# Kernel optimization log

Measured on AMD Instinct MI355X. Metric: run time of the kernel, lower is better.

Reference implementation:

```python
import jax, jax.numpy as jnp
import numpy as np

EPS = 1e-8  # torch.nn.CosineSimilarity default eps


def _cosine_sim(a, b):
    # cosine similarity along channel dim (axis=1), matching torch semantics:
    # dot / (max(||a||, eps) * max(||b||, eps))
    na = jnp.maximum(jnp.sqrt(jnp.sum(a * a, axis=1)), EPS)
    nb = jnp.maximum(jnp.sqrt(jnp.sum(b * b, axis=1)), EPS)
    return jnp.sum(a * b, axis=1) / (na * nb)  # [B, T]


def setup_inputs() -> dict:
    key = jax.random.key(0)
    k1, k2, k3 = jax.random.split(key, 3)
    B, C, T, O, K = 8, 512, 4096, 512, 3
    feature = jax.random.normal(k1, (B, C, T), dtype=jnp.float32)
    embedding = jax.random.normal(k2, (B, C, T), dtype=jnp.float32)
    weight = jax.random.normal(k3, (O, C, K), dtype=jnp.float32) * 0.05
    return {"feature": feature, "embedding": embedding, "weight": weight}


def reference(feature, embedding, weight):
    B, C, T = feature.shape
    O = weight.shape[0]
    K = 3  # kernel_size is structurally 3 in this module

    # shifted embeddings with zero padding (left / right neighbors)
    emb_l = jnp.pad(embedding[:, :, :-1], ((0, 0), (0, 0), (1, 0)))
    emb_r = jnp.pad(embedding[:, :, 1:], ((0, 0), (0, 0), (0, 1)))
    sim = jnp.stack(
        [_cosine_sim(embedding, emb_l),
         _cosine_sim(embedding, embedding),
         _cosine_sim(embedding, emb_r)],
        axis=1,
    )  # [B, 3, T]

    # tile: first C rows = sim_l, next C = sim_c, last C = sim_r -> [B, 3C, T]
    att = jnp.repeat(sim, C, axis=1)

    # im2col (nn.Unfold with kernel (3,1), padding (1,0)): channel-major layout
    f_pad = jnp.pad(feature, ((0, 0), (0, 0), (1, 1)))  # [B, C, T+2]
    inp_unf = jnp.stack([f_pad[:, :, k:k + T] for k in range(K)], axis=2)
    inp_unf = inp_unf.reshape(B, C * K, T)  # row index = c*3 + k (torch unfold order)

    w_flat = weight.reshape(O, C * K)
    # out[b,o,t] = sum_i (inp_unf * att)[b,i,t] * w_flat[o,i]
    out = jnp.einsum('bit,oi->bot', inp_unf * att, w_flat)
    return out
```

## Files before the change

### kernel.cpp

```cpp
#include <hip/hip_runtime.h>
#include <hip/hip_bf16.h>
#include <stdint.h>

#define B_ 8
#define C_ 512
#define T_ 4096
#define O_ 512
#define KP_ 1728
#define EPS_ 1e-8f

#define BM 256
#define BN 128
#define FTP_ROWS 4104

#define LDS_A_USH 16384
#define LDS_B_USH 8192
#define LDS_BUF_USH 24576
#define LDS_BYTES (3 * LDS_BUF_USH * 2)

typedef unsigned short ushort_t;
typedef __attribute__((ext_vector_type(4))) float f32x4;
typedef __attribute__((ext_vector_type(8))) short bf16x8;

__device__ __forceinline__ ushort_t f2bf(float f) {
  union { float f; uint32_t u; } x; x.f = f;
  uint32_t u = x.u;
  uint32_t r = (u + 0x7FFFu + ((u >> 16) & 1u)) >> 16;
  return (ushort_t)r;
}

#define GLOAD16(gsrc, ldst) \
  __builtin_amdgcn_global_load_lds((const __attribute__((address_space(1))) unsigned int*)(gsrc), \
                                   (__attribute__((address_space(3))) unsigned int*)(ldst), 16, 0, 0)

__global__ void sim_reduce_kernel(const float* __restrict__ emb,
                                  float* __restrict__ nn_out,
                                  float* __restrict__ dl_out) {
  const int b = blockIdx.y;
  const int t0 = (blockIdx.x * 64 + threadIdx.x) * 4;
  const int cty = threadIdx.y;
  float nn0=0.f,nn1=0.f,nn2=0.f,nn3=0.f;
  float dl0=0.f,dl1=0.f,dl2=0.f,dl3=0.f;
  const float* base = emb + (size_t)b * C_ * T_;
  for (int c = cty * 128; c < cty * 128 + 128; ++c) {
    const float* row = base + (size_t)c * T_;
    float4 v = *(const float4*)(row + t0);
    float el = (t0 > 0) ? row[t0 - 1] : 0.f;
    nn0 += v.x*v.x; nn1 += v.y*v.y; nn2 += v.z*v.z; nn3 += v.w*v.w;
    dl0 += v.x*el;  dl1 += v.y*v.x; dl2 += v.z*v.y; dl3 += v.w*v.z;
  }
  __shared__ float red[4][64*8];
  float* myr = &red[cty][threadIdx.x * 8];
  if (cty != 0) {
    myr[0]=nn0; myr[1]=nn1; myr[2]=nn2; myr[3]=nn3;
    myr[4]=dl0; myr[5]=dl1; myr[6]=dl2; myr[7]=dl3;
  }
  __syncthreads();
  if (cty == 0) {
    for (int q = 1; q < 4; ++q) {
      float* r = &red[q][threadIdx.x * 8];
      nn0+=r[0]; nn1+=r[1]; nn2+=r[2]; nn3+=r[3];
      dl0+=r[4]; dl1+=r[5]; dl2+=r[6]; dl3+=r[7];
    }
    float* nb = nn_out + (size_t)b * T_ + t0;
    float* db = dl_out + (size_t)b * T_ + t0;
    nb[0]=nn0; nb[1]=nn1; nb[2]=nn2; nb[3]=nn3;
    db[0]=dl0; db[1]=dl1; db[2]=dl2; db[3]=dl3;
  }
}

__global__ void sim_finalize_kernel(const float* __restrict__ nn,
                                    const float* __restrict__ dl,
                                    float* __restrict__ sim) {
  const int idx = blockIdx.x * 256 + threadIdx.x;
  if (idx >= B_ * T_) return;
  const int b = idx >> 12;
  const int t = idx & (T_ - 1);
  const float* nnb = nn + (size_t)b * T_;
  const float* dlb = dl + (size_t)b * T_;
  float nncur = nnb[t];
  float ncur = fmaxf(sqrtf(nncur), EPS_);
  float sc = nncur / (ncur * ncur);
  float sl = 0.f, sr = 0.f;
  if (t > 0) {
    float np = fmaxf(sqrtf(nnb[t - 1]), EPS_);
    sl = dlb[t] / (ncur * np);
  }
  if (t < T_ - 1) {
    float nx = fmaxf(sqrtf(nnb[t + 1]), EPS_);
    sr = dlb[t + 1] / (ncur * nx);
  }
  float* simb = sim + (size_t)b * 3 * T_;
  simb[t] = sl;
  simb[T_ + t] = sc;
  simb[2 * T_ + t] = sr;
}

__global__ void wperm_kernel(const float* __restrict__ w, ushort_t* __restrict__ wbf) {
  const int idx = blockIdx.x * 256 + threadIdx.x;
  if (idx >= O_ * KP_) return;
  const int o = idx / KP_;
  const int p = idx - o * KP_;
  const int g = p / 576; const int r = p - g * 576;
  const int k = r / 192; const int j = r - k * 192;
  const int c_lo = (512 * g - k + 2) / 3;
  const int c_hi = (512 * g + 511 - k) / 3;
  const int c = (c_lo & ~7) + j;
  float v = (c >= c_lo && c <= c_hi) ? w[((size_t)o * C_ + c) * 3 + k] : 0.f;
  wbf[idx] = f2bf(v);
}

__global__ void zero_pads_kernel(ushort_t* __restrict__ Ftp) {
  const int b = blockIdx.x;
  const int rsel = blockIdx.y;
  const int row = (rsel == 0) ? 0 : (rsel == 1 ? T_ + 1 : T_ + 2);
  uint4* dst = (uint4*)(Ftp + ((size_t)b * FTP_ROWS + row) * 512);
  if (threadIdx.x < 64) dst[threadIdx.x] = make_uint4(0, 0, 0, 0);
}

__global__ void transpose_kernel(const float* __restrict__ feat, ushort_t* __restrict__ Ftp) {
  const int b = blockIdx.z;
  const int c0 = blockIdx.y * 64;
  const int t0 = blockIdx.x * 64;
  __shared__ ushort_t LT[64 * 72];
  const int tid = threadIdx.x;
  {
    const int cl = tid >> 2;
    const int tq = (tid & 3) * 16;
    const float* src = feat + ((size_t)b * C_ + c0 + cl) * T_ + t0 + tq;
    for (int q = 0; q < 4; ++q) {
      float4 v = *(const float4*)(src + q * 4);
      const int t = tq + q * 4;
      LT[(t + 0) * 72 + cl] = f2bf(v.x);
      LT[(t + 1) * 72 + cl] = f2bf(v.y);
      LT[(t + 2) * 72 + cl] = f2bf(v.z);
      LT[(t + 3) * 72 + cl] = f2bf(v.w);
    }
  }
  __syncthreads();
  {
    const int tl = tid >> 2;
    const int cq = (tid & 3) * 16;
    ushort_t* dst = Ftp + ((size_t)b * FTP_ROWS + t0 + tl + 1) * 512 + c0 + cq;
    *(uint4*)(dst) = *(const uint4*)&LT[tl * 72 + cq];
    *(uint4*)(dst + 8) = *(const uint4*)&LT[tl * 72 + cq + 8];
  }
}

__global__ __launch_bounds__(512, 2)
void conv_gemm_kernel(const ushort_t* __restrict__ Ftp,
                      const ushort_t* __restrict__ wbf,
                      const float* __restrict__ sim,
                      float* __restrict__ out) {
  extern __shared__ ushort_t lds[];

  const int b = blockIdx.z;
  const int oBase = blockIdx.y * BM;
  const int tBase = blockIdx.x * BN;

  const int tid = threadIdx.x;
  const int lane = tid & 63;
  const int wid = tid >> 6;
  const int wm = wid >> 1;
  const int wn = wid & 1;
  const int llo = lane & 15, lhi = lane >> 4;

  const int rbase = wid * 8 + (lane >> 3);
  const int sw = (((lane & 7) ^ ((lane >> 3) & 7)) << 3);

  const ushort_t* ftpB = Ftp + (size_t)b * FTP_ROWS * 512;
  const float* simB = sim + (size_t)b * 3 * T_;

  float sv[3][4];
#pragma unroll
  for (int g = 0; g < 3; ++g)
#pragma unroll
    for (int n = 0; n < 4; ++n) {
      sv[g][n] = simB[g * T_ + tBase + wn * 64 + n * 16 + llo];
      asm volatile("" : "+v"(sv[g][n]));
    }

  f32x4 cacc[4][4], oacc[4][4];
  const f32x4 vzero = {0.f, 0.f, 0.f, 0.f};
#pragma unroll
  for (int m = 0; m < 4; ++m)
#pragma unroll
    for (int n = 0; n < 4; ++n) { cacc[m][n] = vzero; oacc[m][n] = vzero; }

  auto STAGE = [&](int s2, int p) {
    const int g = s2 / 9, r = s2 - g * 9, k = r / 3, jb = r - k * 3;
    const int c_lo = (512 * g - k + 2) / 3;
    const int c_st = c_lo & ~7;
    const ushort_t* aS = wbf + (size_t)(oBase + rbase) * KP_ + s2 * 64 + sw;
    const ushort_t* bS = ftpB + (size_t)(tBase + rbase + k) * 512 + c_st + jb * 64 + sw;
    ushort_t* Ad = lds + p * LDS_BUF_USH + wid * 512;
    ushort_t* Bd = lds + p * LDS_BUF_USH + LDS_A_USH + wid * 512;
#pragma unroll
    for (int i = 0; i < 4; ++i)
      GLOAD16(aS + (size_t)i * 64 * KP_, Ad + i * 4096);
#pragma unroll
    for (int i = 0; i < 2; ++i)
      GLOAD16(bS + (size_t)i * 64 * 512, Bd + i * 4096);
  };

  STAGE(0, 0); STAGE(1, 1); STAGE(2, 2);

#pragma unroll
  for (int s = 0; s < 27; ++s) {
    if (s <= 24)      { asm volatile("s_waitcnt vmcnt(12)" ::: "memory"); }
    else if (s == 25) { asm volatile("s_waitcnt vmcnt(6)" ::: "memory"); }
    else              { asm volatile("s_waitcnt vmcnt(0)" ::: "memory"); }
    __builtin_amdgcn_s_barrier();
    asm volatile("" ::: "memory");

    const int p = s % 3;
    const ushort_t* As = lds + p * LDS_BUF_USH;
    const ushort_t* Bs = As + LDS_A_USH;
#pragma unroll
    for (int h = 0; h < 2; ++h) {
      bf16x8 af[4], bfv[4];
#pragma unroll
      for (int m = 0; m < 4; ++m) {
        const int row = wm * 64 + m * 16 + llo;
        af[m] = *(const bf16x8*)&As[row * 64 + (((h * 4 + lhi) ^ (llo & 7)) << 3)];
      }
#pragma unroll
      for (int n = 0; n < 4; ++n) {
        const int row = wn * 64 + n * 16 + llo;
        bfv[n] = *(const bf16x8*)&Bs[row * 64 + (((h * 4 + lhi) ^ (llo & 7)) << 3)];
      }
      __builtin_amdgcn_s_setprio(1);
#pragma unroll
      for (int m = 0; m < 4; ++m)
#pragma unroll
        for (int n = 0; n < 4; ++n)
          cacc[m][n] = __builtin_amdgcn_mfma_f32_16x16x32_bf16(af[m], bfv[n], cacc[m][n], 0, 0, 0);
      __builtin_amdgcn_s_setprio(0);
    }

    __builtin_amdgcn_sched_barrier(0);
    asm volatile("" ::: "memory");
    __builtin_amdgcn_s_barrier();
    asm volatile("" ::: "memory");

    if (s + 3 < 27) STAGE(s + 3, p);

    if (s == 8 || s == 17 || s == 26) {
      const int g = s / 9;
#pragma unroll
      for (int n = 0; n < 4; ++n) {
        const float sc = sv[g][n];
#pragma unroll
        for (int m = 0; m < 4; ++m) {
          oacc[m][n] += sc * cacc[m][n];
          cacc[m][n] = vzero;
        }
      }
    }
  }

  float* outB = out + ((size_t)b * O_ + oBase) * T_ + tBase;
#pragma unroll
  for (int m = 0; m < 4; ++m) {
    const int r0 = wm * 64 + m * 16 + lhi * 4;
#pragma unroll
    for (int n = 0; n < 4; ++n) {
      const int cg = wn * 64 + n * 16 + llo;
#pragma unroll
      for (int r = 0; r < 4; ++r)
        outB[(size_t)(r0 + r) * T_ + cg] = oacc[m][n][r];
    }
  }
}

extern "C" void kernel_launch(void* const* d_in, const int* in_sizes, int n_in,
                              void* d_out, int out_size, void* d_ws, size_t ws_size,
                              hipStream_t stream) {
  const float* feature   = (const float*)d_in[0];
  const float* embedding = (const float*)d_in[1];
  const float* weight    = (const float*)d_in[2];
  float* out = (float*)d_out;

  float* ws  = (float*)d_ws;
  float* nn  = ws;
  float* dl  = nn + (size_t)B_ * T_;
  float* sim = dl + (size_t)B_ * T_;
  ushort_t* wbf = (ushort_t*)(sim + (size_t)3 * B_ * T_);
  ushort_t* Ftp = wbf + (size_t)O_ * KP_;

  (void)hipFuncSetAttribute((const void*)conv_gemm_kernel,
                            hipFuncAttributeMaxDynamicSharedMemorySize, LDS_BYTES);

  zero_pads_kernel<<<dim3(B_, 3), 64, 0, stream>>>(Ftp);
  sim_reduce_kernel<<<dim3(T_ / 256, B_), dim3(64, 4), 0, stream>>>(embedding, nn, dl);
  sim_finalize_kernel<<<dim3((B_ * T_) / 256), 256, 0, stream>>>(nn, dl, sim);
  wperm_kernel<<<dim3((O_ * KP_ + 255) / 256), 256, 0, stream>>>(weight, wbf);
  transpose_kernel<<<dim3(T_ / 64, C_ / 64, B_), 256, 0, stream>>>(feature, Ftp);
  conv_gemm_kernel<<<dim3(T_ / BN, O_ / BM, B_), 512, LDS_BYTES, stream>>>(Ftp, wbf, sim, out);
}
```

Measured before the change: 118.0 us.

## Split GEMM stages into half-K ring buffer with single barrier, merge prep kernels

The conv GEMM main loop now stages half-K (32-wide) slices into a 4-slot LDS ring instead of full 64-wide slices in 3 buffers. Each phase issues the next global-to-LDS prefetch right after its fragment reads and needs only one barrier, so loads overlap with MFMA and synchronisation stalls shrink. The swizzle is re-derived for 32-column rows. The sim finalize and weight permute kernels are merged into one launch, and pad zeroing moves into extra transpose blocks, cutting launch count. The risks are more barriers per K step and LDS bank conflicts under the new swizzle.

Result: faster. 115.4 us (-2.2%).

```diff
diff --git a/kernel.cpp b/kernel.cpp
--- a/kernel.cpp
+++ b/kernel.cpp
@@ -13,10 +13,8 @@
 #define BN 128
 #define FTP_ROWS 4104
 
-#define LDS_A_USH 16384
-#define LDS_B_USH 8192
-#define LDS_BUF_USH 24576
-#define LDS_BYTES (3 * LDS_BUF_USH * 2)
+#define RING_USH 12288
+#define LDS_BYTES (4 * RING_USH * 2)
 
 typedef unsigned short ushort_t;
 typedef __attribute__((ext_vector_type(4))) float f32x4;
@@ -69,61 +67,60 @@
   }
 }
 
-__global__ void sim_finalize_kernel(const float* __restrict__ nn,
-                                    const float* __restrict__ dl,
-                                    float* __restrict__ sim) {
-  const int idx = blockIdx.x * 256 + threadIdx.x;
-  if (idx >= B_ * T_) return;
-  const int b = idx >> 12;
-  const int t = idx & (T_ - 1);
-  const float* nnb = nn + (size_t)b * T_;
-  const float* dlb = dl + (size_t)b * T_;
-  float nncur = nnb[t];
-  float ncur = fmaxf(sqrtf(nncur), EPS_);
-  float sc = nncur / (ncur * ncur);
-  float sl = 0.f, sr = 0.f;
-  if (t > 0) {
-    float np = fmaxf(sqrtf(nnb[t - 1]), EPS_);
-    sl = dlb[t] / (ncur * np);
-  }
-  if (t < T_ - 1) {
-    float nx = fmaxf(sqrtf(nnb[t + 1]), EPS_);
-    sr = dlb[t + 1] / (ncur * nx);
-  }
-  float* simb = sim + (size_t)b * 3 * T_;
-  simb[t] = sl;
-  simb[T_ + t] = sc;
-  simb[2 * T_ + t] = sr;
-}
-
-__global__ void wperm_kernel(const float* __restrict__ w, ushort_t* __restrict__ wbf) {
-  const int idx = blockIdx.x * 256 + threadIdx.x;
-  if (idx >= O_ * KP_) return;
-  const int o = idx / KP_;
-  const int p = idx - o * KP_;
-  const int g = p / 576; const int r = p - g * 576;
-  const int k = r / 192; const int j = r - k * 192;
-  const int c_lo = (512 * g - k + 2) / 3;
-  const int c_hi = (512 * g + 511 - k) / 3;
-  const int c = (c_lo & ~7) + j;
-  float v = (c >= c_lo && c <= c_hi) ? w[((size_t)o * C_ + c) * 3 + k] : 0.f;
-  wbf[idx] = f2bf(v);
-}
-
-__global__ void zero_pads_kernel(ushort_t* __restrict__ Ftp) {
-  const int b = blockIdx.x;
-  const int rsel = blockIdx.y;
-  const int row = (rsel == 0) ? 0 : (rsel == 1 ? T_ + 1 : T_ + 2);
-  uint4* dst = (uint4*)(Ftp + ((size_t)b * FTP_ROWS + row) * 512);
-  if (threadIdx.x < 64) dst[threadIdx.x] = make_uint4(0, 0, 0, 0);
+__global__ void prep_small_kernel(const float* __restrict__ nn,
+                                  const float* __restrict__ dl,
+                                  float* __restrict__ sim,
+                                  const float* __restrict__ w,
+                                  ushort_t* __restrict__ wbf) {
+  const int bid = blockIdx.x;
+  if (bid < 128) {
+    const int idx = bid * 256 + threadIdx.x;
+    const int b = idx >> 12;
+    const int t = idx & (T_ - 1);
+    const float* nnb = nn + (size_t)b * T_;
+    const float* dlb = dl + (size_t)b * T_;
+    float nncur = nnb[t];
+    float ncur = fmaxf(sqrtf(nncur), EPS_);
+    float sc = nncur / (ncur * ncur);
+    float sl = 0.f, sr = 0.f;
+    if (t > 0) {
+      float np = fmaxf(sqrtf(nnb[t - 1]), EPS_);
+      sl = dlb[t] / (ncur * np);
+    }
+    if (t < T_ - 1) {
+      float nx = fmaxf(sqrtf(nnb[t + 1]), EPS_);
+      sr = dlb[t + 1] / (ncur * nx);
+    }
+    float* simb = sim + (size_t)b * 3 * T_;
+    simb[t] = sl;
+    simb[T_ + t] = sc;
+    simb[2 * T_ + t] = sr;
+  } else {
+    const int idx = (bid - 128) * 256 + threadIdx.x;
+    if (idx >= O_ * KP_) return;
+    const int o = idx / KP_;
+    const int p = idx - o * KP_;
+    const int g = p / 576; const int r = p - g * 576;
+    const int k = r / 192; const int j = r - k * 192;
+    const int c_lo = (512 * g - k + 2) / 3;
+    const int c_hi = (512 * g + 511 - k) / 3;
+    const int c = (c_lo & ~7) + j;
+    float v = (c >= c_lo && c <= c_hi) ? w[((size_t)o * C_ + c) * 3 + k] : 0.f;
+    wbf[idx] = f2bf(v);
+  }
 }
 
 __global__ void transpose_kernel(const float* __restrict__ feat, ushort_t* __restrict__ Ftp) {
   const int b = blockIdx.z;
   const int c0 = blockIdx.y * 64;
+  const int tid = threadIdx.x;
+  if (blockIdx.x == T_ / 64) {
+    if (tid < 64)        Ftp[((size_t)b * FTP_ROWS + 0) * 512 + c0 + tid] = 0;
+    else if (tid < 128)  Ftp[((size_t)b * FTP_ROWS + T_ + 1) * 512 + c0 + (tid - 64)] = 0;
+    return;
+  }
   const int t0 = blockIdx.x * 64;
   __shared__ ushort_t LT[64 * 72];
-  const int tid = threadIdx.x;
   {
     const int cl = tid >> 2;
     const int tq = (tid & 3) * 16;
@@ -165,8 +162,10 @@
   const int wn = wid & 1;
   const int llo = lane & 15, lhi = lane >> 4;
 
-  const int rbase = wid * 8 + (lane >> 3);
-  const int sw = (((lane & 7) ^ ((lane >> 3) & 7)) << 3);
+  const int rdsw = ((lhi ^ ((llo >> 1) & 3)) << 3);
+  const int gch = ((lane & 3) ^ ((lane >> 3) & 3)) << 3;
+  const int arow = wid * 32 + (lane >> 2);
+  const int brow = wid * 16 + (lane >> 2);
 
   const ushort_t* ftpB = Ftp + (size_t)b * FTP_ROWS * 512;
   const float* simB = sim + (size_t)b * 3 * T_;
@@ -179,6 +178,7 @@
       sv[g][n] = simB[g * T_ + tBase + wn * 64 + n * 16 + llo];
       asm volatile("" : "+v"(sv[g][n]));
     }
+  asm volatile("s_waitcnt vmcnt(0)" ::: "memory");
 
   f32x4 cacc[4][4], oacc[4][4];
   const f32x4 vzero = {0.f, 0.f, 0.f, 0.f};
@@ -187,64 +187,56 @@
 #pragma unroll
     for (int n = 0; n < 4; ++n) { cacc[m][n] = vzero; oacc[m][n] = vzero; }
 
-  auto STAGE = [&](int s2, int p) {
+  auto STAGE = [&](int u) {
+    const int s2 = u >> 1, h = u & 1;
     const int g = s2 / 9, r = s2 - g * 9, k = r / 3, jb = r - k * 3;
-    const int c_lo = (512 * g - k + 2) / 3;
-    const int c_st = c_lo & ~7;
-    const ushort_t* aS = wbf + (size_t)(oBase + rbase) * KP_ + s2 * 64 + sw;
-    const ushort_t* bS = ftpB + (size_t)(tBase + rbase + k) * 512 + c_st + jb * 64 + sw;
-    ushort_t* Ad = lds + p * LDS_BUF_USH + wid * 512;
-    ushort_t* Bd = lds + p * LDS_BUF_USH + LDS_A_USH + wid * 512;
-#pragma unroll
-    for (int i = 0; i < 4; ++i)
-      GLOAD16(aS + (size_t)i * 64 * KP_, Ad + i * 4096);
-#pragma unroll
-    for (int i = 0; i < 2; ++i)
-      GLOAD16(bS + (size_t)i * 64 * 512, Bd + i * 4096);
+    const int c_st = ((512 * g - k + 2) / 3) & ~7;
+    ushort_t* ring = lds + (u & 3) * RING_USH;
+    const ushort_t* aS = wbf + (size_t)(oBase + arow) * KP_ + s2 * 64 + h * 32 + gch;
+    GLOAD16(aS, ring + wid * 1024);
+    GLOAD16(aS + (size_t)16 * KP_, ring + wid * 1024 + 512);
+    const ushort_t* bS = ftpB + (size_t)(tBase + brow + k) * 512 + c_st + jb * 64 + h * 32 + gch;
+    GLOAD16(bS, ring + 8192 + wid * 512);
   };
 
-  STAGE(0, 0); STAGE(1, 1); STAGE(2, 2);
-
-#pragma unroll
-  for (int s = 0; s < 27; ++s) {
-    if (s <= 24)      { asm volatile("s_waitcnt vmcnt(12)" ::: "memory"); }
-    else if (s == 25) { asm volatile("s_waitcnt vmcnt(6)" ::: "memory"); }
+  auto PHASE = [&](int u, int vm) {
+    if (vm == 6)      { asm volatile("s_waitcnt vmcnt(6)" ::: "memory"); }
+    else if (vm == 3) { asm volatile("s_waitcnt vmcnt(3)" ::: "memory"); }
     else              { asm volatile("s_waitcnt vmcnt(0)" ::: "memory"); }
     __builtin_amdgcn_s_barrier();
     asm volatile("" ::: "memory");
 
-    const int p = s % 3;
-    const ushort_t* As = lds + p * LDS_BUF_USH;
-    const ushort_t* Bs = As + LDS_A_USH;
-#pragma unroll
-    for (int h = 0; h < 2; ++h) {
-      bf16x8 af[4], bfv[4];
-#pragma unroll
-      for (int m = 0; m < 4; ++m) {
-        const int row = wm * 64 + m * 16 + llo;
-        af[m] = *(const bf16x8*)&As[row * 64 + (((h * 4 + lhi) ^ (llo & 7)) << 3)];
-      }
-#pragma unroll
-      for (int n = 0; n < 4; ++n) {
-        const int row = wn * 64 + n * 16 + llo;
-        bfv[n] = *(const bf16x8*)&Bs[row * 64 + (((h * 4 + lhi) ^ (llo & 7)) << 3)];
-      }
-      __builtin_amdgcn_s_setprio(1);
-#pragma unroll
-      for (int m = 0; m < 4; ++m)
-#pragma unroll
-        for (int n = 0; n < 4; ++n)
-          cacc[m][n] = __builtin_amdgcn_mfma_f32_16x16x32_bf16(af[m], bfv[n], cacc[m][n], 0, 0, 0);
-      __builtin_amdgcn_s_setprio(0);
-    }
-
+    const ushort_t* Ah = lds + (u & 3) * RING_USH;
+    const ushort_t* Bh = Ah + 8192;
+    bf16x8 af[4], bfv[4];
+#pragma unroll
+    for (int m = 0; m < 4; ++m)
+      af[m] = *(const bf16x8*)&Ah[(wm * 64 + m * 16 + llo) * 32 + rdsw];
+#pragma unroll
+    for (int n = 0; n < 4; ++n)
+      bfv[n] = *(const bf16x8*)&Bh[(wn * 64 + n * 16 + llo) * 32 + rdsw];
+
+    if (u + 3 < 54) STAGE(u + 3);
+
+    __builtin_amdgcn_s_setprio(1);
+#pragma unroll
+    for (int m = 0; m < 4; ++m)
+#pragma unroll
+      for (int n = 0; n < 4; ++n)
+        cacc[m][n] = __builtin_amdgcn_mfma_f32_16x16x32_bf16(af[m], bfv[n], cacc[m][n], 0, 0, 0);
+    __builtin_amdgcn_s_setprio(0);
+
+    asm volatile("s_waitcnt lgkmcnt(0)" ::: "memory");
     __builtin_amdgcn_sched_barrier(0);
-    asm volatile("" ::: "memory");
-    __builtin_amdgcn_s_barrier();
-    asm volatile("" ::: "memory");
-
-    if (s + 3 < 27) STAGE(s + 3, p);
-
+  };
+
+  STAGE(0); STAGE(1); STAGE(2);
+
+#pragma unroll
+  for (int s = 0; s < 27; ++s) {
+    const int u0 = 2 * s, u1 = 2 * s + 1;
+    PHASE(u0, u0 < 52 ? 6 : 3);
+    PHASE(u1, u1 < 52 ? 6 : 0);
     if (s == 8 || s == 17 || s == 26) {
       const int g = s / 9;
 #pragma unroll
@@ -291,10 +283,8 @@
   (void)hipFuncSetAttribute((const void*)conv_gemm_kernel,
                             hipFuncAttributeMaxDynamicSharedMemorySize, LDS_BYTES);
 
-  zero_pads_kernel<<<dim3(B_, 3), 64, 0, stream>>>(Ftp);
   sim_reduce_kernel<<<dim3(T_ / 256, B_), dim3(64, 4), 0, stream>>>(embedding, nn, dl);
-  sim_finalize_kernel<<<dim3((B_ * T_) / 256), 256, 0, stream>>>(nn, dl, sim);
-  wperm_kernel<<<dim3((O_ * KP_ + 255) / 256), 256, 0, stream>>>(weight, wbf);
-  transpose_kernel<<<dim3(T_ / 64, C_ / 64, B_), 256, 0, stream>>>(feature, Ftp);
+  prep_small_kernel<<<dim3(128 + (O_ * KP_ + 255) / 256), 256, 0, stream>>>(nn, dl, sim, weight, wbf);
+  transpose_kernel<<<dim3(T_ / 64 + 1, C_ / 64, B_), 256, 0, stream>>>(feature, Ftp);
   conv_gemm_kernel<<<dim3(T_ / BN, O_ / BM, B_), 512, LDS_BYTES, stream>>>(Ftp, wbf, sim, out);
 }
```
